# Performance work log

Measured on AMD Instinct MI355X. Metric: run time of the kernel, lower is better.

## Reference

```python
import jax, jax.numpy as jnp
import numpy as np

B, S, F, RANK = 8, 4096, 1024, 64


def gram_schmidt(P):
    """Sequential Gram-Schmidt on columns of P (F, R) -> orthogonal (unnormalized) columns.
    Matches vizbert's orth_tensor: v_i = p_i - sum_{j<i} ((u_j . v)/(u_j . u_j)) u_j.
    Each step vectorizes the inner projection loop as one matmul (u_j are mutually
    orthogonal, so sequential-update and batched coefficients are equal in exact math)."""
    us = [P[:, 0]]
    for i in range(1, P.shape[1]):
        U = jnp.stack(us, axis=1)                 # (F, i)
        sq = jnp.sum(U * U, axis=0)               # (i,)
        v = P[:, i]
        coeff = (U.T @ v) / sq                    # (i,)
        us.append(v - U @ coeff)
    return jnp.stack(us, axis=1)                  # (F, R)


def setup_inputs() -> dict:
    key = jax.random.key(0)
    k1, k2 = jax.random.split(key)
    hidden_states = jax.random.normal(k1, (B, S, F), dtype=jnp.float32)
    # probe params initialized uniform(-0.05, 0.05), stacked to (num_features, rank)
    probe = jax.random.uniform(k2, (F, RANK), minval=-0.05, maxval=0.05, dtype=jnp.float32)
    return {"hidden_states": hidden_states, "probe": probe}


def reference(hidden_states, probe):
    # orth_probe: Gram-Schmidt orthogonalized probe columns (orthogonalize=True)
    U = gram_schmidt(probe)                       # (F, R), orthogonal columns
    sq = jnp.sum(U * U, axis=0)                   # (R,) squared norms

    # normalize=True: remember per-token norms before projection
    old_norms = jnp.linalg.norm(hidden_states, axis=2, keepdims=True)  # (B, S, 1)
    # mask_first=True: remember first-token states
    first_state = hidden_states[:, 0]             # (B, F)

    # full_batch_gs: subtract projection onto each probe direction.
    # Because U's columns are orthogonal, the sequential per-column subtraction
    # equals one fused projection: h - U (U^T h / ||u||^2).
    coeffs = jnp.einsum('bsf,fr->bsr', hidden_states, U) / sq
    h = hidden_states - jnp.einsum('bsr,fr->bsf', coeffs, U)

    # normalize=True: rescale back to the original per-token norm
    new_norms = jnp.linalg.norm(h, axis=2, keepdims=True)
    h = h / new_norms * old_norms

    # mask_first=True: restore the first token untouched
    h = h.at[:, 0].set(first_state)
    return h
```

## Files before the change

kernel.cpp:

```cpp
#include <hip/hip_runtime.h>


typedef __attribute__((ext_vector_type(8))) short bf16x8;
typedef __attribute__((ext_vector_type(4))) float f32x4;

#define MFMA_B16(a, b, c) __builtin_amdgcn_mfma_f32_16x16x32_bf16((a), (b), (c), 0, 0, 0)

__device__ __forceinline__ unsigned short bf16bits(float x) {
  union { float f; unsigned u; } v; v.f = x;
  return (unsigned short)((v.u + 0x7fffu + ((v.u >> 16) & 1u)) >> 16);
}
__device__ __forceinline__ unsigned pack2(float a, float b) {
  return (unsigned)bf16bits(a) | ((unsigned)bf16bits(b) << 16);
}
__device__ __forceinline__ bf16x8 cvt8(const float* p) {
  f32x4 v0 = *(const f32x4*)p;
  f32x4 v1 = *(const f32x4*)(p + 4);
  bf16x8 r;
  r[0] = (short)bf16bits(v0[0]); r[1] = (short)bf16bits(v0[1]);
  r[2] = (short)bf16bits(v0[2]); r[3] = (short)bf16bits(v0[3]);
  r[4] = (short)bf16bits(v1[0]); r[5] = (short)bf16bits(v1[1]);
  r[6] = (short)bf16bits(v1[2]); r[7] = (short)bf16bits(v1[3]);
  return r;
}

__global__ void pp_gram(const float* __restrict__ P, float* __restrict__ partial) {
  __shared__ float Pl[64][68];
  const int tid = threadIdx.x, ch = blockIdx.x;
  #pragma unroll
  for (int u = 0; u < 4; ++u) {
    const int f = tid >> 2, r = (tid & 3) * 16 + 4 * u;
    *(f32x4*)&Pl[f][r] = *(const f32x4*)(P + (size_t)(ch * 64 + f) * 64 + r);
  }
  __syncthreads();
  const int a0 = (tid >> 4) * 4, b0 = (tid & 15) * 4;
  f32x4 acc[4];
  #pragma unroll
  for (int i = 0; i < 4; ++i) acc[i] = (f32x4){0.f, 0.f, 0.f, 0.f};
  for (int k = 0; k < 64; ++k) {
    f32x4 av = *(const f32x4*)&Pl[k][a0];
    f32x4 bv = *(const f32x4*)&Pl[k][b0];
    #pragma unroll
    for (int i = 0; i < 4; ++i) acc[i] += av[i] * bv;
  }
  #pragma unroll
  for (int i = 0; i < 4; ++i)
    *(f32x4*)(partial + (size_t)ch * 4096 + (size_t)(a0 + i) * 64 + b0) = acc[i];
}

__global__ void pp_invert(const float* __restrict__ partial, float* __restrict__ W) {
  __shared__ float A[64][68];
  const int tid = threadIdx.x;
  const int i = tid >> 2, q = tid & 3, q16 = (tid & 3) * 16;
  #pragma unroll
  for (int u = 0; u < 4; ++u) {
    f32x4 s = (f32x4){0.f, 0.f, 0.f, 0.f};
    const int off = i * 64 + q16 + 4 * u;
    for (int p = 0; p < 16; ++p) s += *(const f32x4*)(partial + (size_t)p * 4096 + off);
    *(f32x4*)&A[i][q16 + 4 * u] = s;
  }
  __syncthreads();
  for (int k = 0; k < 64; ++k) {
    const float d = 1.0f / A[k][k];
    const float f = A[i][k];
    f32x4 prs[4], cur[4];
    #pragma unroll
    for (int u = 0; u < 4; ++u) {
      prs[u] = *(const f32x4*)&A[k][q16 + 4 * u];
      cur[u] = *(const f32x4*)&A[i][q16 + 4 * u];
    }
    __syncthreads();
    const int kl = k - q16;
    #pragma unroll
    for (int u = 0; u < 4; ++u) {
      f32x4 pv = prs[u] * d;
      if (kl >= u * 4 && kl < u * 4 + 4) { pv[kl - u * 4] = d; cur[u][kl - u * 4] = 0.f; }
      f32x4 res = (i == k) ? pv : (cur[u] - f * pv);
      *(f32x4*)&A[i][q16 + 4 * u] = res;
    }
    __syncthreads();
  }
  #pragma unroll
  for (int u = 0; u < 4; ++u)
    *(f32x4*)(W + (size_t)i * 64 + q16 + 4 * u) = *(const f32x4*)&A[i][q16 + 4 * u];
}

__global__ void pp_pack(const float* __restrict__ P, unsigned short* __restrict__ Ptb,
                        unsigned short* __restrict__ Pb) {
  const int g = blockIdx.x * 256 + threadIdx.x;
  const int flat = g * 4;
  const int f = flat >> 6, r = flat & 63;
  f32x4 v = *(const f32x4*)(P + flat);
  unsigned short b[4];
  #pragma unroll
  for (int u = 0; u < 4; ++u) b[u] = bf16bits(v[u]);
  unsigned lo = (unsigned)b[0] | ((unsigned)b[1] << 16);
  unsigned hi = (unsigned)b[2] | ((unsigned)b[3] << 16);
  *(unsigned long long*)(Pb + flat) = (unsigned long long)lo | ((unsigned long long)hi << 32);
  #pragma unroll
  for (int u = 0; u < 4; ++u) Ptb[(size_t)(r + u) * 1024 + f] = b[u];
}

__global__ __launch_bounds__(256, 2) void pp_main(
    const float* __restrict__ H, const unsigned short* __restrict__ Ptb,
    const unsigned short* __restrict__ Pb, const float* __restrict__ W,
    float* __restrict__ out) {
  __shared__ unsigned short Ha[64][136];
  __shared__ float Yl[64][68];
  __shared__ float Cl[64][68];
  __shared__ unsigned short Wl[64][72];
  __shared__ float rowsq[64], dotv[64], scalev[64];

  const int tid = threadIdx.x;
  const int lane = tid & 63, wid = tid >> 6;
  const int c16 = lane & 15, quad = lane >> 4;
  const int strip = wid * 16;
  const int srow = tid >> 2, sg = tid & 3;
  const long row0 = (long)blockIdx.x * 64;

  if (tid < 64) { rowsq[tid] = 0.f; dotv[tid] = 0.f; }
  for (int u = tid; u < 4096; u += 256) Wl[u >> 6][u & 63] = bf16bits(W[u]);

  f32x4 accY[4];
  #pragma unroll
  for (int t = 0; t < 4; ++t) accY[t] = (f32x4){0.f, 0.f, 0.f, 0.f};

  float sqacc = 0.f;
  const float* hrow = H + (row0 + srow) * 1024 + sg * 32;

  for (int ch = 0; ch < 8; ++ch) {
    const float* hp = hrow + ch * 128;
    #pragma unroll
    for (int u = 0; u < 8; ++u) {
      f32x4 v = *(const f32x4*)(hp + 4 * u);
      sqacc += v[0] * v[0] + v[1] * v[1] + v[2] * v[2] + v[3] * v[3];
      unsigned lo = pack2(v[0], v[1]), hi = pack2(v[2], v[3]);
      *(unsigned long long*)&Ha[srow][sg * 32 + 4 * u] =
          (unsigned long long)lo | ((unsigned long long)hi << 32);
    }
    __syncthreads();
    #pragma unroll
    for (int it = 0; it < 4; ++it) {
      bf16x8 a = *(const bf16x8*)&Ha[strip + c16][it * 32 + quad * 8];
      const unsigned short* bp = Ptb + (size_t)c16 * 1024 + ch * 128 + it * 32 + quad * 8;
      #pragma unroll
      for (int t = 0; t < 4; ++t) {
        bf16x8 b = *(const bf16x8*)(bp + (size_t)t * 16 * 1024);
        accY[t] = MFMA_B16(a, b, accY[t]);
      }
    }
    __syncthreads();
  }
  atomicAdd(&rowsq[srow], sqacc);
  #pragma unroll
  for (int t = 0; t < 4; ++t)
    #pragma unroll
    for (int r = 0; r < 4; ++r)
      Yl[strip + quad * 4 + r][t * 16 + c16] = accY[t][r];
  __syncthreads();

  f32x4 accC[4];
  #pragma unroll
  for (int t = 0; t < 4; ++t) accC[t] = (f32x4){0.f, 0.f, 0.f, 0.f};
  #pragma unroll
  for (int kk = 0; kk < 2; ++kk) {
    bf16x8 a = cvt8(&Yl[strip + c16][kk * 32 + quad * 8]);
    #pragma unroll
    for (int t = 0; t < 4; ++t) {
      bf16x8 b = *(const bf16x8*)&Wl[t * 16 + c16][kk * 32 + quad * 8];
      accC[t] = MFMA_B16(a, b, accC[t]);
    }
  }
  #pragma unroll
  for (int t = 0; t < 4; ++t)
    #pragma unroll
    for (int r = 0; r < 4; ++r) Cl[strip + quad * 4 + r][t * 16 + c16] = accC[t][r];
  __syncthreads();

  {
    float d = 0.f;
    #pragma unroll
    for (int u = 0; u < 4; ++u) {
      f32x4 yv = *(const f32x4*)&Yl[srow][sg * 16 + 4 * u];
      f32x4 cv = *(const f32x4*)&Cl[srow][sg * 16 + 4 * u];
      d += yv[0] * cv[0] + yv[1] * cv[1] + yv[2] * cv[2] + yv[3] * cv[3];
    }
    atomicAdd(&dotv[srow], d);
  }
  __syncthreads();
  if (tid < 64) {
    float o2 = rowsq[tid];
    float n2 = fmaxf(o2 - dotv[tid], 1e-30f);
    scalev[tid] = sqrtf(o2 / n2);
  }
  __syncthreads();

  bf16x8 ca0 = cvt8(&Cl[strip + c16][quad * 8]);
  bf16x8 ca1 = cvt8(&Cl[strip + c16][32 + quad * 8]);
  float sc[4]; long rg[4]; bool fs[4];
  #pragma unroll
  for (int r = 0; r < 4; ++r) {
    const int m = strip + quad * 4 + r;
    sc[r] = scalev[m];
    rg[r] = row0 + m;
    fs[r] = ((rg[r] & 4095) == 0);
  }
  for (int ft = 0; ft < 64; ++ft) {
    const unsigned short* bp = Pb + (size_t)(ft * 16 + c16) * 64 + quad * 8;
    bf16x8 b0 = *(const bf16x8*)bp;
    bf16x8 b1 = *(const bf16x8*)(bp + 32);
    f32x4 acc = (f32x4){0.f, 0.f, 0.f, 0.f};
    acc = MFMA_B16(ca0, b0, acc);
    acc = MFMA_B16(ca1, b1, acc);
    const int f = ft * 16 + c16;
    #pragma unroll
    for (int r = 0; r < 4; ++r) {
      const long idx = rg[r] * 1024 + f;
      const float h = H[idx];
      out[idx] = fs[r] ? h : (h - acc[r]) * sc[r];
    }
  }
}

extern "C" void kernel_launch(void* const* d_in, const int* in_sizes, int n_in,
                              void* d_out, int out_size, void* d_ws, size_t ws_size,
                              hipStream_t stream) {
  const float* H = (const float*)d_in[0];
  const float* P = (const float*)d_in[1];
  float* out = (float*)d_out;
  float* ws = (float*)d_ws;
  float* W = ws;
  float* partial = ws + 4096;
  unsigned short* Ptb = (unsigned short*)(ws + 4096 + 16 * 4096);
  unsigned short* Pb = Ptb + 65536;

  pp_gram<<<16, 256, 0, stream>>>(P, partial);
  pp_invert<<<1, 256, 0, stream>>>(partial, W);
  pp_pack<<<64, 256, 0, stream>>>(P, Ptb, Pb);
  pp_main<<<512, 256, 0, stream>>>(H, Ptb, Pb, W, out);
}
```

Measured before the change: 325.6 us.

## Fuse pack into gram, single-wave invert, register-direct H loads in main

Folds the bf16 packing of the probe into the Gram kernel, which removes one launch. The Gauss-Jordan inversion now runs as a single 64-thread wave with wave barriers in place of block syncs, and writes W already converted to bf16. The main kernel loads H straight into MFMA A-operand registers with double buffering instead of staging it through LDS. It computes row norms and the Y·C dot with shuffles rather than LDS atomics, which drops most __syncthreads, and keeps Y and C in bf16 in LDS. The risks are higher register pressure and bf16 rounding in the norm-correction dot product.

```diff
diff --git a/kernel.cpp b/kernel.cpp
--- a/kernel.cpp
+++ b/kernel.cpp
@@ -10,21 +10,9 @@
   union { float f; unsigned u; } v; v.f = x;
   return (unsigned short)((v.u + 0x7fffu + ((v.u >> 16) & 1u)) >> 16);
 }
-__device__ __forceinline__ unsigned pack2(float a, float b) {
-  return (unsigned)bf16bits(a) | ((unsigned)bf16bits(b) << 16);
-}
-__device__ __forceinline__ bf16x8 cvt8(const float* p) {
-  f32x4 v0 = *(const f32x4*)p;
-  f32x4 v1 = *(const f32x4*)(p + 4);
-  bf16x8 r;
-  r[0] = (short)bf16bits(v0[0]); r[1] = (short)bf16bits(v0[1]);
-  r[2] = (short)bf16bits(v0[2]); r[3] = (short)bf16bits(v0[3]);
-  r[4] = (short)bf16bits(v1[0]); r[5] = (short)bf16bits(v1[1]);
-  r[6] = (short)bf16bits(v1[2]); r[7] = (short)bf16bits(v1[3]);
-  return r;
-}
-
-__global__ void pp_gram(const float* __restrict__ P, float* __restrict__ partial) {
+
+__global__ void pp_gram(const float* __restrict__ P, float* __restrict__ partial,
+                        unsigned short* __restrict__ Ptb, unsigned short* __restrict__ Pb) {
   __shared__ float Pl[64][68];
   const int tid = threadIdx.x, ch = blockIdx.x;
   #pragma unroll
@@ -33,6 +21,28 @@
     *(f32x4*)&Pl[f][r] = *(const f32x4*)(P + (size_t)(ch * 64 + f) * 64 + r);
   }
   __syncthreads();
+  {
+    const int f = tid >> 2, r0 = (tid & 3) * 16;
+    bf16x8 w0, w1;
+    #pragma unroll
+    for (int j = 0; j < 8; ++j) {
+      w0[j] = (short)bf16bits(Pl[f][r0 + j]);
+      w1[j] = (short)bf16bits(Pl[f][r0 + 8 + j]);
+    }
+    *(bf16x8*)(Pb + (size_t)(ch * 64 + f) * 64 + r0) = w0;
+    *(bf16x8*)(Pb + (size_t)(ch * 64 + f) * 64 + r0 + 8) = w1;
+  }
+  {
+    const int r = tid >> 2, f0 = (tid & 3) * 16;
+    bf16x8 w0, w1;
+    #pragma unroll
+    for (int j = 0; j < 8; ++j) {
+      w0[j] = (short)bf16bits(Pl[f0 + j][r]);
+      w1[j] = (short)bf16bits(Pl[f0 + 8 + j][r]);
+    }
+    *(bf16x8*)(Ptb + (size_t)r * 1024 + ch * 64 + f0) = w0;
+    *(bf16x8*)(Ptb + (size_t)r * 1024 + ch * 64 + f0 + 8) = w1;
+  }
   const int a0 = (tid >> 4) * 4, b0 = (tid & 15) * 4;
   f32x4 acc[4];
   #pragma unroll
@@ -48,163 +58,161 @@
     *(f32x4*)(partial + (size_t)ch * 4096 + (size_t)(a0 + i) * 64 + b0) = acc[i];
 }
 
-__global__ void pp_invert(const float* __restrict__ partial, float* __restrict__ W) {
+__global__ void pp_invert(const float* __restrict__ partial, unsigned short* __restrict__ Wb) {
   __shared__ float A[64][68];
-  const int tid = threadIdx.x;
-  const int i = tid >> 2, q = tid & 3, q16 = (tid & 3) * 16;
-  #pragma unroll
-  for (int u = 0; u < 4; ++u) {
+  const int i = threadIdx.x;
+  #pragma unroll
+  for (int c = 0; c < 16; ++c) {
     f32x4 s = (f32x4){0.f, 0.f, 0.f, 0.f};
-    const int off = i * 64 + q16 + 4 * u;
-    for (int p = 0; p < 16; ++p) s += *(const f32x4*)(partial + (size_t)p * 4096 + off);
-    *(f32x4*)&A[i][q16 + 4 * u] = s;
+    #pragma unroll 4
+    for (int p = 0; p < 16; ++p)
+      s += *(const f32x4*)(partial + (size_t)p * 4096 + (size_t)i * 64 + c * 4);
+    *(f32x4*)&A[i][c * 4] = s;
   }
   __syncthreads();
   for (int k = 0; k < 64; ++k) {
     const float d = 1.0f / A[k][k];
-    const float f = A[i][k];
-    f32x4 prs[4], cur[4];
-    #pragma unroll
-    for (int u = 0; u < 4; ++u) {
-      prs[u] = *(const f32x4*)&A[k][q16 + 4 * u];
-      cur[u] = *(const f32x4*)&A[i][q16 + 4 * u];
-    }
-    __syncthreads();
-    const int kl = k - q16;
-    #pragma unroll
-    for (int u = 0; u < 4; ++u) {
-      f32x4 pv = prs[u] * d;
-      if (kl >= u * 4 && kl < u * 4 + 4) { pv[kl - u * 4] = d; cur[u][kl - u * 4] = 0.f; }
-      f32x4 res = (i == k) ? pv : (cur[u] - f * pv);
-      *(f32x4*)&A[i][q16 + 4 * u] = res;
-    }
-    __syncthreads();
-  }
-  #pragma unroll
-  for (int u = 0; u < 4; ++u)
-    *(f32x4*)(W + (size_t)i * 64 + q16 + 4 * u) = *(const f32x4*)&A[i][q16 + 4 * u];
-}
-
-__global__ void pp_pack(const float* __restrict__ P, unsigned short* __restrict__ Ptb,
-                        unsigned short* __restrict__ Pb) {
-  const int g = blockIdx.x * 256 + threadIdx.x;
-  const int flat = g * 4;
-  const int f = flat >> 6, r = flat & 63;
-  f32x4 v = *(const f32x4*)(P + flat);
-  unsigned short b[4];
-  #pragma unroll
-  for (int u = 0; u < 4; ++u) b[u] = bf16bits(v[u]);
-  unsigned lo = (unsigned)b[0] | ((unsigned)b[1] << 16);
-  unsigned hi = (unsigned)b[2] | ((unsigned)b[3] << 16);
-  *(unsigned long long*)(Pb + flat) = (unsigned long long)lo | ((unsigned long long)hi << 32);
-  #pragma unroll
-  for (int u = 0; u < 4; ++u) Ptb[(size_t)(r + u) * 1024 + f] = b[u];
+    const float fi = A[i][k];
+    #pragma unroll
+    for (int c = 0; c < 16; ++c) {
+      f32x4 pr = *(const f32x4*)&A[k][c * 4];
+      f32x4 cur = *(const f32x4*)&A[i][c * 4];
+      f32x4 res;
+      #pragma unroll
+      for (int e = 0; e < 4; ++e) {
+        const bool isp = (c * 4 + e) == k;
+        const float pv = isp ? d : pr[e] * d;
+        const float cu = isp ? 0.f : cur[e];
+        res[e] = (i == k) ? pv : (cu - fi * pv);
+      }
+      *(f32x4*)&A[i][c * 4] = res;
+    }
+    __builtin_amdgcn_wave_barrier();
+  }
+  #pragma unroll
+  for (int c = 0; c < 8; ++c) {
+    bf16x8 w;
+    #pragma unroll
+    for (int j = 0; j < 8; ++j) w[j] = (short)bf16bits(A[i][c * 8 + j]);
+    *(bf16x8*)(Wb + (size_t)i * 64 + c * 8) = w;
+  }
+}
+
+__device__ __forceinline__ void ld_chunk(const float* __restrict__ hp, int ch, f32x4* v) {
+  #pragma unroll
+  for (int it = 0; it < 4; ++it) {
+    v[2 * it] = *(const f32x4*)(hp + ch * 128 + it * 32);
+    v[2 * it + 1] = *(const f32x4*)(hp + ch * 128 + it * 32 + 4);
+  }
+}
+
+__device__ __forceinline__ void comp_chunk(const f32x4* v, const unsigned short* __restrict__ bp0,
+                                           int ch, f32x4* accY, float& sqacc) {
+  #pragma unroll
+  for (int it = 0; it < 4; ++it) {
+    const f32x4 v0 = v[2 * it], v1 = v[2 * it + 1];
+    sqacc += v0[0] * v0[0] + v0[1] * v0[1] + v0[2] * v0[2] + v0[3] * v0[3] +
+             v1[0] * v1[0] + v1[1] * v1[1] + v1[2] * v1[2] + v1[3] * v1[3];
+    bf16x8 a;
+    a[0] = (short)bf16bits(v0[0]); a[1] = (short)bf16bits(v0[1]);
+    a[2] = (short)bf16bits(v0[2]); a[3] = (short)bf16bits(v0[3]);
+    a[4] = (short)bf16bits(v1[0]); a[5] = (short)bf16bits(v1[1]);
+    a[6] = (short)bf16bits(v1[2]); a[7] = (short)bf16bits(v1[3]);
+    const unsigned short* bp = bp0 + ch * 128 + it * 32;
+    #pragma unroll
+    for (int t = 0; t < 4; ++t) {
+      bf16x8 b = *(const bf16x8*)(bp + (size_t)t * 16 * 1024);
+      accY[t] = MFMA_B16(a, b, accY[t]);
+    }
+  }
 }
 
 __global__ __launch_bounds__(256, 2) void pp_main(
     const float* __restrict__ H, const unsigned short* __restrict__ Ptb,
-    const unsigned short* __restrict__ Pb, const float* __restrict__ W,
+    const unsigned short* __restrict__ Pb, const unsigned short* __restrict__ Wb,
     float* __restrict__ out) {
-  __shared__ unsigned short Ha[64][136];
-  __shared__ float Yl[64][68];
-  __shared__ float Cl[64][68];
-  __shared__ unsigned short Wl[64][72];
-  __shared__ float rowsq[64], dotv[64], scalev[64];
+  __shared__ __align__(16) unsigned short Yl[64][72];
+  __shared__ __align__(16) unsigned short Cl[64][72];
+  __shared__ __align__(16) unsigned short Wl[64][72];
 
   const int tid = threadIdx.x;
   const int lane = tid & 63, wid = tid >> 6;
   const int c16 = lane & 15, quad = lane >> 4;
   const int strip = wid * 16;
-  const int srow = tid >> 2, sg = tid & 3;
   const long row0 = (long)blockIdx.x * 64;
 
-  if (tid < 64) { rowsq[tid] = 0.f; dotv[tid] = 0.f; }
-  for (int u = tid; u < 4096; u += 256) Wl[u >> 6][u & 63] = bf16bits(W[u]);
+  #pragma unroll
+  for (int g = 0; g < 2; ++g) {
+    const int u = tid + g * 256;
+    *(bf16x8*)&Wl[u >> 3][(u & 7) * 8] = *(const bf16x8*)(Wb + (size_t)u * 8);
+  }
+  __syncthreads();
 
   f32x4 accY[4];
   #pragma unroll
   for (int t = 0; t < 4; ++t) accY[t] = (f32x4){0.f, 0.f, 0.f, 0.f};
-
   float sqacc = 0.f;
-  const float* hrow = H + (row0 + srow) * 1024 + sg * 32;
-
-  for (int ch = 0; ch < 8; ++ch) {
-    const float* hp = hrow + ch * 128;
-    #pragma unroll
-    for (int u = 0; u < 8; ++u) {
-      f32x4 v = *(const f32x4*)(hp + 4 * u);
-      sqacc += v[0] * v[0] + v[1] * v[1] + v[2] * v[2] + v[3] * v[3];
-      unsigned lo = pack2(v[0], v[1]), hi = pack2(v[2], v[3]);
-      *(unsigned long long*)&Ha[srow][sg * 32 + 4 * u] =
-          (unsigned long long)lo | ((unsigned long long)hi << 32);
-    }
-    __syncthreads();
-    #pragma unroll
-    for (int it = 0; it < 4; ++it) {
-      bf16x8 a = *(const bf16x8*)&Ha[strip + c16][it * 32 + quad * 8];
-      const unsigned short* bp = Ptb + (size_t)c16 * 1024 + ch * 128 + it * 32 + quad * 8;
-      #pragma unroll
-      for (int t = 0; t < 4; ++t) {
-        bf16x8 b = *(const bf16x8*)(bp + (size_t)t * 16 * 1024);
-        accY[t] = MFMA_B16(a, b, accY[t]);
-      }
-    }
-    __syncthreads();
-  }
-  atomicAdd(&rowsq[srow], sqacc);
+  const float* hp = H + (row0 + strip + c16) * 1024 + quad * 8;
+  const unsigned short* bp0 = Ptb + (size_t)c16 * 1024 + quad * 8;
+  {
+    f32x4 va[8], vb[8];
+    ld_chunk(hp, 0, va);
+    #pragma unroll
+    for (int c2 = 0; c2 < 4; ++c2) {
+      ld_chunk(hp, 2 * c2 + 1, vb);
+      comp_chunk(va, bp0, 2 * c2, accY, sqacc);
+      if (c2 < 3) ld_chunk(hp, 2 * c2 + 2, va);
+      comp_chunk(vb, bp0, 2 * c2 + 1, accY, sqacc);
+    }
+  }
+
+  sqacc += __shfl_xor(sqacc, 16);
+  sqacc += __shfl_xor(sqacc, 32);
+
   #pragma unroll
   for (int t = 0; t < 4; ++t)
     #pragma unroll
     for (int r = 0; r < 4; ++r)
-      Yl[strip + quad * 4 + r][t * 16 + c16] = accY[t][r];
-  __syncthreads();
+      Yl[strip + quad * 4 + r][t * 16 + c16] = bf16bits(accY[t][r]);
 
   f32x4 accC[4];
   #pragma unroll
   for (int t = 0; t < 4; ++t) accC[t] = (f32x4){0.f, 0.f, 0.f, 0.f};
   #pragma unroll
   for (int kk = 0; kk < 2; ++kk) {
-    bf16x8 a = cvt8(&Yl[strip + c16][kk * 32 + quad * 8]);
+    bf16x8 a = *(const bf16x8*)&Yl[strip + c16][kk * 32 + quad * 8];
     #pragma unroll
     for (int t = 0; t < 4; ++t) {
       bf16x8 b = *(const bf16x8*)&Wl[t * 16 + c16][kk * 32 + quad * 8];
       accC[t] = MFMA_B16(a, b, accC[t]);
     }
   }
+
   #pragma unroll
   for (int t = 0; t < 4; ++t)
     #pragma unroll
-    for (int r = 0; r < 4; ++r) Cl[strip + quad * 4 + r][t * 16 + c16] = accC[t][r];
-  __syncthreads();
-
-  {
-    float d = 0.f;
-    #pragma unroll
-    for (int u = 0; u < 4; ++u) {
-      f32x4 yv = *(const f32x4*)&Yl[srow][sg * 16 + 4 * u];
-      f32x4 cv = *(const f32x4*)&Cl[srow][sg * 16 + 4 * u];
-      d += yv[0] * cv[0] + yv[1] * cv[1] + yv[2] * cv[2] + yv[3] * cv[3];
-    }
-    atomicAdd(&dotv[srow], d);
-  }
-  __syncthreads();
-  if (tid < 64) {
-    float o2 = rowsq[tid];
-    float n2 = fmaxf(o2 - dotv[tid], 1e-30f);
-    scalev[tid] = sqrtf(o2 / n2);
-  }
-  __syncthreads();
-
-  bf16x8 ca0 = cvt8(&Cl[strip + c16][quad * 8]);
-  bf16x8 ca1 = cvt8(&Cl[strip + c16][32 + quad * 8]);
+    for (int r = 0; r < 4; ++r)
+      Cl[strip + quad * 4 + r][t * 16 + c16] = bf16bits(accC[t][r]);
+
   float sc[4]; long rg[4]; bool fs[4];
   #pragma unroll
   for (int r = 0; r < 4; ++r) {
-    const int m = strip + quad * 4 + r;
-    sc[r] = scalev[m];
-    rg[r] = row0 + m;
+    float dd = accY[0][r] * accC[0][r] + accY[1][r] * accC[1][r] +
+               accY[2][r] * accC[2][r] + accY[3][r] * accC[3][r];
+    dd += __shfl_xor(dd, 1);
+    dd += __shfl_xor(dd, 2);
+    dd += __shfl_xor(dd, 4);
+    dd += __shfl_xor(dd, 8);
+    const float o2 = __shfl(sqacc, quad * 4 + r);
+    const float n2 = fmaxf(o2 - dd, 1e-30f);
+    sc[r] = sqrtf(o2 / n2);
+    rg[r] = row0 + strip + quad * 4 + r;
     fs[r] = ((rg[r] & 4095) == 0);
   }
+
+  bf16x8 ca0 = *(const bf16x8*)&Cl[strip + c16][quad * 8];
+  bf16x8 ca1 = *(const bf16x8*)&Cl[strip + c16][32 + quad * 8];
+  #pragma unroll 4
   for (int ft = 0; ft < 64; ++ft) {
     const unsigned short* bp = Pb + (size_t)(ft * 16 + c16) * 64 + quad * 8;
     bf16x8 b0 = *(const bf16x8*)bp;
@@ -228,14 +236,12 @@
   const float* H = (const float*)d_in[0];
   const float* P = (const float*)d_in[1];
   float* out = (float*)d_out;
-  float* ws = (float*)d_ws;
-  float* W = ws;
-  float* partial = ws + 4096;
-  unsigned short* Ptb = (unsigned short*)(ws + 4096 + 16 * 4096);
+  float* partial = (float*)d_ws;
+  unsigned short* Wb = (unsigned short*)(partial + 16 * 4096);
+  unsigned short* Ptb = Wb + 4096;
   unsigned short* Pb = Ptb + 65536;
 
-  pp_gram<<<16, 256, 0, stream>>>(P, partial);
-  pp_invert<<<1, 256, 0, stream>>>(partial, W);
-  pp_pack<<<64, 256, 0, stream>>>(P, Ptb, Pb);
-  pp_main<<<512, 256, 0, stream>>>(H, Ptb, Pb, W, out);
-}
+  pp_gram<<<16, 256, 0, stream>>>(P, partial, Ptb, Pb);
+  pp_invert<<<1, 64, 0, stream>>>(partial, Wb);
+  pp_main<<<512, 256, 0, stream>>>(H, Ptb, Pb, Wb, out);
+}
```

Measured after the change: 388.8 us. 19.4% more time.

## Fuse prep kernels, pre-swizzle MFMA operands, and coalesce output stores via LDS

Applied to the files above, without the earlier changes.

The three prep kernels become one, which uses an atomic completion counter so block 0 inverts the Gram matrix after all partial sums land. P, P^T and W are stored pre-swizzled in MFMA fragment order, so the main kernel loads operands with contiguous per-lane vector reads. Intermediates are kept in bf16 in LDS, and the row dot-product reduction uses register shuffles instead of shared atomics. The final projection is staged through LDS so H reads and output writes become 16-byte coalesced vectors instead of scalar strided accesses. The spin-wait across blocks relies on all 16 blocks being co-resident, and the extra bf16 rounding of Y and C may add numerical error.

```diff
diff --git a/kernel.cpp b/kernel.cpp
--- a/kernel.cpp
+++ b/kernel.cpp
@@ -10,48 +10,75 @@
   union { float f; unsigned u; } v; v.f = x;
   return (unsigned short)((v.u + 0x7fffu + ((v.u >> 16) & 1u)) >> 16);
 }
-__device__ __forceinline__ unsigned pack2(float a, float b) {
-  return (unsigned)bf16bits(a) | ((unsigned)bf16bits(b) << 16);
-}
-__device__ __forceinline__ bf16x8 cvt8(const float* p) {
-  f32x4 v0 = *(const f32x4*)p;
-  f32x4 v1 = *(const f32x4*)(p + 4);
-  bf16x8 r;
-  r[0] = (short)bf16bits(v0[0]); r[1] = (short)bf16bits(v0[1]);
-  r[2] = (short)bf16bits(v0[2]); r[3] = (short)bf16bits(v0[3]);
-  r[4] = (short)bf16bits(v1[0]); r[5] = (short)bf16bits(v1[1]);
-  r[6] = (short)bf16bits(v1[2]); r[7] = (short)bf16bits(v1[3]);
-  return r;
-}
-
-__global__ void pp_gram(const float* __restrict__ P, float* __restrict__ partial) {
+
+__global__ void pp_prep(const float* __restrict__ P, float* __restrict__ partial,
+                        unsigned short* __restrict__ Ptf, unsigned short* __restrict__ Pbf,
+                        unsigned short* __restrict__ Wf, unsigned int* __restrict__ done) {
   __shared__ float Pl[64][68];
-  const int tid = threadIdx.x, ch = blockIdx.x;
+  __shared__ float A[64][68];
+  const int tid = threadIdx.x, b = blockIdx.x;
   #pragma unroll
   for (int u = 0; u < 4; ++u) {
     const int f = tid >> 2, r = (tid & 3) * 16 + 4 * u;
-    *(f32x4*)&Pl[f][r] = *(const f32x4*)(P + (size_t)(ch * 64 + f) * 64 + r);
-  }
-  __syncthreads();
-  const int a0 = (tid >> 4) * 4, b0 = (tid & 15) * 4;
-  f32x4 acc[4];
-  #pragma unroll
-  for (int i = 0; i < 4; ++i) acc[i] = (f32x4){0.f, 0.f, 0.f, 0.f};
-  for (int k = 0; k < 64; ++k) {
-    f32x4 av = *(const f32x4*)&Pl[k][a0];
-    f32x4 bv = *(const f32x4*)&Pl[k][b0];
-    #pragma unroll
-    for (int i = 0; i < 4; ++i) acc[i] += av[i] * bv;
-  }
-  #pragma unroll
-  for (int i = 0; i < 4; ++i)
-    *(f32x4*)(partial + (size_t)ch * 4096 + (size_t)(a0 + i) * 64 + b0) = acc[i];
-}
-
-__global__ void pp_invert(const float* __restrict__ partial, float* __restrict__ W) {
-  __shared__ float A[64][68];
-  const int tid = threadIdx.x;
-  const int i = tid >> 2, q = tid & 3, q16 = (tid & 3) * 16;
+    *(f32x4*)&Pl[f][r] = *(const f32x4*)(P + (size_t)(b * 64 + f) * 64 + r);
+  }
+  __syncthreads();
+
+  #pragma unroll
+  for (int u = 0; u < 2; ++u) {
+    const int flat = tid + 256 * u;
+    const int lf = flat >> 6, lane = flat & 63;
+    const int c16 = lane & 15, quad = lane >> 4;
+    const int it_loc = lf >> 2, t = lf & 3;
+    const int flb = it_loc * 32 + quad * 8;
+    bf16x8 w;
+    #pragma unroll
+    for (int e = 0; e < 8; ++e) w[e] = (short)bf16bits(Pl[flb + e][t * 16 + c16]);
+    const int gidx = ((b >> 1) * 4 + 2 * (b & 1) + it_loc) * 4 + t;
+    *(bf16x8*)(Ptf + ((size_t)gidx * 64 + lane) * 8) = w;
+  }
+  #pragma unroll
+  for (int u = 0; u < 2; ++u) {
+    const int flat = tid + 256 * u;
+    const int lf = flat >> 6, lane = flat & 63;
+    const int c16 = lane & 15, quad = lane >> 4;
+    const int t2 = lf >> 1, j = lf & 1;
+    f32x4 p0 = *(const f32x4*)&Pl[t2 * 16 + c16][j * 32 + quad * 8];
+    f32x4 p1 = *(const f32x4*)&Pl[t2 * 16 + c16][j * 32 + quad * 8 + 4];
+    bf16x8 w;
+    #pragma unroll
+    for (int e = 0; e < 4; ++e) { w[e] = (short)bf16bits(p0[e]); w[4 + e] = (short)bf16bits(p1[e]); }
+    const int gidx = b * 8 + t2 * 2 + j;
+    *(bf16x8*)(Pbf + ((size_t)gidx * 64 + lane) * 8) = w;
+  }
+
+  {
+    const int a0 = (tid >> 4) * 4, b0 = (tid & 15) * 4;
+    f32x4 acc[4];
+    #pragma unroll
+    for (int i = 0; i < 4; ++i) acc[i] = (f32x4){0.f, 0.f, 0.f, 0.f};
+    for (int k = 0; k < 64; ++k) {
+      f32x4 av = *(const f32x4*)&Pl[k][a0];
+      f32x4 bv = *(const f32x4*)&Pl[k][b0];
+      #pragma unroll
+      for (int i = 0; i < 4; ++i) acc[i] += av[i] * bv;
+    }
+    #pragma unroll
+    for (int i = 0; i < 4; ++i)
+      *(f32x4*)(partial + (size_t)b * 4096 + (size_t)(a0 + i) * 64 + b0) = acc[i];
+  }
+  __threadfence();
+  __syncthreads();
+  if (tid == 0) atomicAdd(done, 1u);
+  if (b != 0) return;
+
+  if (tid == 0) {
+    while (__hip_atomic_load(done, __ATOMIC_ACQUIRE, __HIP_MEMORY_SCOPE_AGENT) < 16u)
+      __builtin_amdgcn_s_sleep(8);
+  }
+  __syncthreads();
+  __threadfence();
+  const int i = tid >> 2, q16 = (tid & 3) * 16;
   #pragma unroll
   for (int u = 0; u < 4; ++u) {
     f32x4 s = (f32x4){0.f, 0.f, 0.f, 0.f};
@@ -81,82 +108,81 @@
     __syncthreads();
   }
   #pragma unroll
-  for (int u = 0; u < 4; ++u)
-    *(f32x4*)(W + (size_t)i * 64 + q16 + 4 * u) = *(const f32x4*)&A[i][q16 + 4 * u];
-}
-
-__global__ void pp_pack(const float* __restrict__ P, unsigned short* __restrict__ Ptb,
-                        unsigned short* __restrict__ Pb) {
-  const int g = blockIdx.x * 256 + threadIdx.x;
-  const int flat = g * 4;
-  const int f = flat >> 6, r = flat & 63;
-  f32x4 v = *(const f32x4*)(P + flat);
-  unsigned short b[4];
-  #pragma unroll
-  for (int u = 0; u < 4; ++u) b[u] = bf16bits(v[u]);
-  unsigned lo = (unsigned)b[0] | ((unsigned)b[1] << 16);
-  unsigned hi = (unsigned)b[2] | ((unsigned)b[3] << 16);
-  *(unsigned long long*)(Pb + flat) = (unsigned long long)lo | ((unsigned long long)hi << 32);
-  #pragma unroll
-  for (int u = 0; u < 4; ++u) Ptb[(size_t)(r + u) * 1024 + f] = b[u];
+  for (int u = 0; u < 2; ++u) {
+    const int flat = tid + 256 * u;
+    const int lf = flat >> 6, lane = flat & 63;
+    const int c16 = lane & 15, quad = lane >> 4;
+    const int kk = lf >> 2, tf = lf & 3;
+    bf16x8 w;
+    #pragma unroll
+    for (int e = 0; e < 8; ++e) w[e] = (short)bf16bits(A[kk * 32 + quad * 8 + e][tf * 16 + c16]);
+    *(bf16x8*)(Wf + ((size_t)(kk * 4 + tf) * 64 + lane) * 8) = w;
+  }
 }
 
 __global__ __launch_bounds__(256, 2) void pp_main(
-    const float* __restrict__ H, const unsigned short* __restrict__ Ptb,
-    const unsigned short* __restrict__ Pb, const float* __restrict__ W,
+    const float* __restrict__ H, const unsigned short* __restrict__ Ptf,
+    const unsigned short* __restrict__ Pbf, const unsigned short* __restrict__ Wf,
     float* __restrict__ out) {
-  __shared__ unsigned short Ha[64][136];
-  __shared__ float Yl[64][68];
-  __shared__ float Cl[64][68];
-  __shared__ unsigned short Wl[64][72];
-  __shared__ float rowsq[64], dotv[64], scalev[64];
+  __shared__ __align__(16) unsigned short Ha[64][136];
+  __shared__ __align__(16) unsigned short Yl[64][72];
+  __shared__ __align__(16) unsigned short Cl[64][72];
+  __shared__ float rowsqL[64];
+  __shared__ float scalevL[64];
 
   const int tid = threadIdx.x;
   const int lane = tid & 63, wid = tid >> 6;
   const int c16 = lane & 15, quad = lane >> 4;
   const int strip = wid * 16;
-  const int srow = tid >> 2, sg = tid & 3;
   const long row0 = (long)blockIdx.x * 64;
-
-  if (tid < 64) { rowsq[tid] = 0.f; dotv[tid] = 0.f; }
-  for (int u = tid; u < 4096; u += 256) Wl[u >> 6][u & 63] = bf16bits(W[u]);
+  const int sr = tid >> 3;
+  const int sc8 = (tid & 7) * 4;
 
   f32x4 accY[4];
   #pragma unroll
   for (int t = 0; t < 4; ++t) accY[t] = (f32x4){0.f, 0.f, 0.f, 0.f};
-
-  float sqacc = 0.f;
-  const float* hrow = H + (row0 + srow) * 1024 + sg * 32;
+  float sqa0 = 0.f, sqa1 = 0.f;
 
   for (int ch = 0; ch < 8; ++ch) {
-    const float* hp = hrow + ch * 128;
-    #pragma unroll
-    for (int u = 0; u < 8; ++u) {
-      f32x4 v = *(const f32x4*)(hp + 4 * u);
-      sqacc += v[0] * v[0] + v[1] * v[1] + v[2] * v[2] + v[3] * v[3];
-      unsigned lo = pack2(v[0], v[1]), hi = pack2(v[2], v[3]);
-      *(unsigned long long*)&Ha[srow][sg * 32 + 4 * u] =
-          (unsigned long long)lo | ((unsigned long long)hi << 32);
+    #pragma unroll
+    for (int ph = 0; ph < 2; ++ph) {
+      const int row = ph * 32 + sr;
+      const float* hp = H + (row0 + row) * 1024 + ch * 128;
+      #pragma unroll
+      for (int p = 0; p < 4; ++p) {
+        const int col = p * 32 + sc8;
+        f32x4 v = *(const f32x4*)(hp + col);
+        const float d2 = v[0] * v[0] + v[1] * v[1] + v[2] * v[2] + v[3] * v[3];
+        if (ph == 0) sqa0 += d2; else sqa1 += d2;
+        unsigned lo = (unsigned)bf16bits(v[0]) | ((unsigned)bf16bits(v[1]) << 16);
+        unsigned hi = (unsigned)bf16bits(v[2]) | ((unsigned)bf16bits(v[3]) << 16);
+        *(unsigned long long*)&Ha[row][col] =
+            (unsigned long long)lo | ((unsigned long long)hi << 32);
+      }
     }
     __syncthreads();
     #pragma unroll
     for (int it = 0; it < 4; ++it) {
       bf16x8 a = *(const bf16x8*)&Ha[strip + c16][it * 32 + quad * 8];
-      const unsigned short* bp = Ptb + (size_t)c16 * 1024 + ch * 128 + it * 32 + quad * 8;
       #pragma unroll
       for (int t = 0; t < 4; ++t) {
-        bf16x8 b = *(const bf16x8*)(bp + (size_t)t * 16 * 1024);
+        bf16x8 b = *(const bf16x8*)(Ptf + (((size_t)(ch * 4 + it) * 4 + t) * 64 + lane) * 8);
         accY[t] = MFMA_B16(a, b, accY[t]);
       }
     }
     __syncthreads();
   }
-  atomicAdd(&rowsq[srow], sqacc);
+
+  sqa0 += __shfl_xor(sqa0, 1); sqa1 += __shfl_xor(sqa1, 1);
+  sqa0 += __shfl_xor(sqa0, 2); sqa1 += __shfl_xor(sqa1, 2);
+  sqa0 += __shfl_xor(sqa0, 4); sqa1 += __shfl_xor(sqa1, 4);
+  if ((lane & 7) == 0) { rowsqL[sr] = sqa0; rowsqL[sr + 32] = sqa1; }
+
   #pragma unroll
   for (int t = 0; t < 4; ++t)
     #pragma unroll
     for (int r = 0; r < 4; ++r)
-      Yl[strip + quad * 4 + r][t * 16 + c16] = accY[t][r];
+      Yl[strip + quad * 4 + r][t * 16 + c16] = bf16bits(accY[t][r]);
   __syncthreads();
 
   f32x4 accC[4];
@@ -164,61 +190,77 @@
   for (int t = 0; t < 4; ++t) accC[t] = (f32x4){0.f, 0.f, 0.f, 0.f};
   #pragma unroll
   for (int kk = 0; kk < 2; ++kk) {
-    bf16x8 a = cvt8(&Yl[strip + c16][kk * 32 + quad * 8]);
+    bf16x8 a = *(const bf16x8*)&Yl[strip + c16][kk * 32 + quad * 8];
     #pragma unroll
     for (int t = 0; t < 4; ++t) {
-      bf16x8 b = *(const bf16x8*)&Wl[t * 16 + c16][kk * 32 + quad * 8];
+      bf16x8 b = *(const bf16x8*)(Wf + (((size_t)kk * 4 + t) * 64 + lane) * 8);
       accC[t] = MFMA_B16(a, b, accC[t]);
     }
   }
   #pragma unroll
   for (int t = 0; t < 4; ++t)
     #pragma unroll
-    for (int r = 0; r < 4; ++r) Cl[strip + quad * 4 + r][t * 16 + c16] = accC[t][r];
-  __syncthreads();
-
-  {
-    float d = 0.f;
-    #pragma unroll
-    for (int u = 0; u < 4; ++u) {
-      f32x4 yv = *(const f32x4*)&Yl[srow][sg * 16 + 4 * u];
-      f32x4 cv = *(const f32x4*)&Cl[srow][sg * 16 + 4 * u];
-      d += yv[0] * cv[0] + yv[1] * cv[1] + yv[2] * cv[2] + yv[3] * cv[3];
-    }
-    atomicAdd(&dotv[srow], d);
-  }
-  __syncthreads();
-  if (tid < 64) {
-    float o2 = rowsq[tid];
-    float n2 = fmaxf(o2 - dotv[tid], 1e-30f);
-    scalev[tid] = sqrtf(o2 / n2);
-  }
-  __syncthreads();
-
-  bf16x8 ca0 = cvt8(&Cl[strip + c16][quad * 8]);
-  bf16x8 ca1 = cvt8(&Cl[strip + c16][32 + quad * 8]);
-  float sc[4]; long rg[4]; bool fs[4];
+    for (int r = 0; r < 4; ++r)
+      Cl[strip + quad * 4 + r][t * 16 + c16] = bf16bits(accC[t][r]);
+
   #pragma unroll
   for (int r = 0; r < 4; ++r) {
-    const int m = strip + quad * 4 + r;
-    sc[r] = scalev[m];
-    rg[r] = row0 + m;
-    fs[r] = ((rg[r] & 4095) == 0);
-  }
-  for (int ft = 0; ft < 64; ++ft) {
-    const unsigned short* bp = Pb + (size_t)(ft * 16 + c16) * 64 + quad * 8;
-    bf16x8 b0 = *(const bf16x8*)bp;
-    bf16x8 b1 = *(const bf16x8*)(bp + 32);
-    f32x4 acc = (f32x4){0.f, 0.f, 0.f, 0.f};
-    acc = MFMA_B16(ca0, b0, acc);
-    acc = MFMA_B16(ca1, b1, acc);
-    const int f = ft * 16 + c16;
-    #pragma unroll
-    for (int r = 0; r < 4; ++r) {
-      const long idx = rg[r] * 1024 + f;
-      const float h = H[idx];
-      out[idx] = fs[r] ? h : (h - acc[r]) * sc[r];
-    }
+    float dd = accY[0][r] * accC[0][r] + accY[1][r] * accC[1][r] +
+               accY[2][r] * accC[2][r] + accY[3][r] * accC[3][r];
+    dd += __shfl_xor(dd, 1);
+    dd += __shfl_xor(dd, 2);
+    dd += __shfl_xor(dd, 4);
+    dd += __shfl_xor(dd, 8);
+    if (c16 == 0) {
+      const int rowm = strip + quad * 4 + r;
+      const float o2 = rowsqL[rowm];
+      const float n2 = fmaxf(o2 - dd, 1e-30f);
+      scalevL[rowm] = sqrtf(o2 / n2);
+    }
+  }
+
+  bf16x8 ca0 = *(const bf16x8*)&Cl[strip + c16][quad * 8];
+  bf16x8 ca1 = *(const bf16x8*)&Cl[strip + c16][32 + quad * 8];
+  float* Tl = (float*)(&Ha[0][0]) + wid * 1088;
+  const int pr = lane >> 3;
+  const int pc = (lane & 7) * 4;
+  const float scA = scalevL[strip + pr];
+  const float scB = scalevL[strip + 8 + pr];
+  const long growA = row0 + strip + pr;
+  const long growB = growA + 8;
+  const bool fsA = ((growA & 4095) == 0);
+
+  for (int g = 0; g < 16; ++g) {
+    bf16x8 bb[8];
+    #pragma unroll
+    for (int f8 = 0; f8 < 8; ++f8)
+      bb[f8] = *(const bf16x8*)(Pbf + (((size_t)g * 8 + f8) * 64 + lane) * 8);
+    #pragma unroll
+    for (int t2 = 0; t2 < 4; ++t2) {
+      f32x4 acc = (f32x4){0.f, 0.f, 0.f, 0.f};
+      acc = MFMA_B16(ca0, bb[t2 * 2], acc);
+      acc = MFMA_B16(ca1, bb[t2 * 2 + 1], acc);
+      #pragma unroll
+      for (int r = 0; r < 4; ++r)
+        Tl[(quad * 4 + r) * 68 + t2 * 16 + c16] = acc[r];
+    }
+    __builtin_amdgcn_wave_barrier();
+    #pragma unroll
+    for (int s = 0; s < 4; ++s) {
+      const int trow = (s & 1) * 8 + pr;
+      const int fcol = (s >> 1) * 32 + pc;
+      f32x4 tv = *(const f32x4*)&Tl[trow * 68 + fcol];
+      const long grow = (s & 1) ? growB : growA;
+      const float scv = (s & 1) ? scB : scA;
+      const long base = grow * 1024 + g * 64 + fcol;
+      f32x4 h = *(const f32x4*)(H + base);
+      f32x4 o;
+      #pragma unroll
+      for (int e = 0; e < 4; ++e) o[e] = (h[e] - tv[e]) * scv;
+      if ((s & 1) == 0 && fsA) o = h;
+      *(f32x4*)(out + base) = o;
+    }
+    __builtin_amdgcn_wave_barrier();
   }
 }
 
@@ -228,14 +270,13 @@
   const float* H = (const float*)d_in[0];
   const float* P = (const float*)d_in[1];
   float* out = (float*)d_out;
-  float* ws = (float*)d_ws;
-  float* W = ws;
-  float* partial = ws + 4096;
-  unsigned short* Ptb = (unsigned short*)(ws + 4096 + 16 * 4096);
-  unsigned short* Pb = Ptb + 65536;
-
-  pp_gram<<<16, 256, 0, stream>>>(P, partial);
-  pp_invert<<<1, 256, 0, stream>>>(partial, W);
-  pp_pack<<<64, 256, 0, stream>>>(P, Ptb, Pb);
-  pp_main<<<512, 256, 0, stream>>>(H, Ptb, Pb, W, out);
-}
+  float* partial = (float*)d_ws;
+  unsigned short* Ptf = (unsigned short*)(partial + 16 * 4096);
+  unsigned short* Pbf = Ptf + 65536;
+  unsigned short* Wf = Pbf + 65536;
+  unsigned int* done = (unsigned int*)(Wf + 4096);
+
+  hipMemsetAsync(done, 0, sizeof(unsigned int), stream);
+  pp_prep<<<16, 256, 0, stream>>>(P, partial, Ptf, Pbf, Wf, done);
+  pp_main<<<512, 256, 0, stream>>>(H, Ptf, Pbf, Wf, out);
+}
```

After: 347.6 us. +6.7%, slower.
